# Kernel optimization log

Measured on AMD Instinct MI355X. Metric: run time of the kernel, lower is better.

## Reference

```python
import jax, jax.numpy as jnp
import numpy as np


def setup_inputs() -> dict:
    key = jax.random.key(0)
    ks = jax.random.split(key, 7)
    B, T, H = 4, 4096, 1024
    scale = 1.0 / np.sqrt(H)
    states = jax.random.normal(ks[0], (B, T, H), dtype=jnp.float32)
    Wq = jax.random.normal(ks[1], (H, H), dtype=jnp.float32) * scale
    bq = jax.random.normal(ks[2], (H,), dtype=jnp.float32) * 0.01
    Wk = jax.random.normal(ks[3], (H, H), dtype=jnp.float32) * scale
    bk = jax.random.normal(ks[4], (H,), dtype=jnp.float32) * 0.01
    Wv = jax.random.normal(ks[5], (H, H), dtype=jnp.float32) * scale
    bv = jax.random.normal(ks[6], (H,), dtype=jnp.float32) * 0.01
    return {"states": states, "Wq": Wq, "bq": bq, "Wk": Wk, "bk": bk,
            "Wv": Wv, "bv": bv, "window": 8}


def reference(states, Wq, bq, Wk, bk, Wv, bv, window):
    # states: [B, T, H]; torch Linear: y = x @ W.T + b
    B, T, H = states.shape
    W = window + 1  # context length per query (positions t-window .. t)
    q = states @ Wq.T + bq  # [B,T,H]
    k = states @ Wk.T + bk
    v = states @ Wv.T + bv
    # Windowed gather indices: idx[t, w] = t - window + w
    idx = jnp.arange(T)[:, None] + jnp.arange(-window, 1)[None, :]  # [T,W]
    valid = idx >= 0
    idxc = jnp.clip(idx, 0, T - 1)
    kw = k[:, idxc]  # [B,T,W,H]
    vw = v[:, idxc]  # [B,T,W,H]
    scores = jnp.einsum('bth,btwh->btw', q, kw) / jnp.sqrt(jnp.float32(H))
    scores = jnp.where(valid[None, :, :], scores, -jnp.inf)
    attn = jax.nn.softmax(scores, axis=-1)  # [B,T,W]
    out = jnp.einsum('btw,btwh->bth', attn, vw)
    return out
```

## Files before the change

### kernel.cpp

```cpp
#include <hip/hip_runtime.h>
#include <hip/hip_bf16.h>
#include <stdint.h>
#include <math.h>

typedef __attribute__((ext_vector_type(8))) short short8;
typedef __attribute__((ext_vector_type(4))) float f32x4;

#define H_DIM 1024
#define T_SEQ 4096
#define BM 128
#define BN 128
#define BK 32

static __device__ __forceinline__ float bf2f(unsigned short u) {
  union { unsigned int i; float f; } c;
  c.i = ((unsigned int)u) << 16;
  return c.f;
}

static __device__ __forceinline__ unsigned short f2bf(float f) {
  __hip_bfloat16 h = __float2bfloat16(f);
  unsigned short u;
  __builtin_memcpy(&u, &h, 2);
  return u;
}

static __device__ __forceinline__ void gload16(const void* g, void* l) {
  __builtin_amdgcn_global_load_lds(
      (const __attribute__((address_space(1))) void*)g,
      (__attribute__((address_space(3))) void*)l,
      16, 0, 0);
}

__global__ __launch_bounds__(256) void cvt_kernel(
    const float* __restrict__ in, __hip_bfloat16* __restrict__ out, int n8)
{
  int i = blockIdx.x * blockDim.x + threadIdx.x;
  const int stride = gridDim.x * blockDim.x;
  for (; i < n8; i += stride) {
    const float4* p = (const float4*)in + (size_t)i * 2;
    float4 a = p[0], b = p[1];
    short8 o;
    o[0] = (short)f2bf(a.x); o[1] = (short)f2bf(a.y);
    o[2] = (short)f2bf(a.z); o[3] = (short)f2bf(a.w);
    o[4] = (short)f2bf(b.x); o[5] = (short)f2bf(b.y);
    o[6] = (short)f2bf(b.z); o[7] = (short)f2bf(b.w);
    ((short8*)out)[i] = o;
  }
}

__global__ __launch_bounds__(256) void cvt3_kernel(
    const float* __restrict__ i0, const float* __restrict__ i1,
    const float* __restrict__ i2,
    __hip_bfloat16* __restrict__ o0, __hip_bfloat16* __restrict__ o1,
    __hip_bfloat16* __restrict__ o2, int n8)
{
  const float* in = (blockIdx.y == 0) ? i0 : ((blockIdx.y == 1) ? i1 : i2);
  __hip_bfloat16* out = (blockIdx.y == 0) ? o0 : ((blockIdx.y == 1) ? o1 : o2);
  int i = blockIdx.x * blockDim.x + threadIdx.x;
  const int stride = gridDim.x * blockDim.x;
  for (; i < n8; i += stride) {
    const float4* p = (const float4*)in + (size_t)i * 2;
    float4 a = p[0], b = p[1];
    short8 o;
    o[0] = (short)f2bf(a.x); o[1] = (short)f2bf(a.y);
    o[2] = (short)f2bf(a.z); o[3] = (short)f2bf(a.w);
    o[4] = (short)f2bf(b.x); o[5] = (short)f2bf(b.y);
    o[6] = (short)f2bf(b.z); o[7] = (short)f2bf(b.w);
    ((short8*)out)[i] = o;
  }
}

__global__ __launch_bounds__(256) void qkv_gemm_kernel(
    const __hip_bfloat16* __restrict__ X,
    const __hip_bfloat16* __restrict__ Wq,
    const __hip_bfloat16* __restrict__ Wk,
    const __hip_bfloat16* __restrict__ Wv,
    const float* __restrict__ bq,
    const float* __restrict__ bk,
    const float* __restrict__ bv,
    __hip_bfloat16* __restrict__ Qo,
    __hip_bfloat16* __restrict__ Ko,
    __hip_bfloat16* __restrict__ Vo,
    int M)
{
  __shared__ __hip_bfloat16 sA[BM * BK];
  __shared__ __hip_bfloat16 sB[BN * BK];

  const int m0 = blockIdx.x * BM;
  const int ytile = blockIdx.y;
  const int which = ytile >> 3;
  const int n_local = (ytile & 7) * BN;

  const __hip_bfloat16* Wsel = (which == 0) ? Wq : ((which == 1) ? Wk : Wv);
  const float* Bsel          = (which == 0) ? bq : ((which == 1) ? bk : bv);
  __hip_bfloat16* Osel       = (which == 0) ? Qo : ((which == 1) ? Ko : Vo);

  const int tid  = threadIdx.x;
  const int lane = tid & 63;
  const int wv   = tid >> 6;
  const int wm   = (wv >> 1) * 64;
  const int wn   = (wv & 1) * 64;

  f32x4 acc[4][4];
  #pragma unroll
  for (int i = 0; i < 4; ++i)
    #pragma unroll
    for (int j = 0; j < 4; ++j)
      acc[i][j] = (f32x4){0.f, 0.f, 0.f, 0.f};

  const int ar = wm + (lane & 15);
  const int br = wn + (lane & 15);
  const int kq = lane >> 4;

  const int nkt = H_DIM / BK;

  for (int kt = 0; kt < nkt; ++kt) {
    const int k0 = kt * BK;
    #pragma unroll
    for (int i = 0; i < 2; ++i) {
      int idx = i * 256 + tid;
      int row = idx >> 2;
      int ck  = (idx & 3) * 8;
      gload16(X    + (size_t)(m0 + row)      * H_DIM + k0 + ck, (char*)sA + idx * 16);
      gload16(Wsel + (size_t)(n_local + row) * H_DIM + k0 + ck, (char*)sB + idx * 16);
    }
    __syncthreads();

    const short8* pA = (const short8*)sA;
    const short8* pB = (const short8*)sB;
    short8 afrag[4], bfrag[4];
    #pragma unroll
    for (int mi = 0; mi < 4; ++mi)
      afrag[mi] = pA[(ar + mi * 16) * 4 + kq];
    #pragma unroll
    for (int ni = 0; ni < 4; ++ni)
      bfrag[ni] = pB[(br + ni * 16) * 4 + kq];

    #pragma unroll
    for (int mi = 0; mi < 4; ++mi)
      #pragma unroll
      for (int ni = 0; ni < 4; ++ni)
        acc[mi][ni] = __builtin_amdgcn_mfma_f32_16x16x32_bf16(
            afrag[mi], bfrag[ni], acc[mi][ni], 0, 0, 0);

    __syncthreads();
  }

  #pragma unroll
  for (int ni = 0; ni < 4; ++ni) {
    const int col = n_local + wn + ni * 16 + (lane & 15);
    const float bias = Bsel[col];
    #pragma unroll
    for (int mi = 0; mi < 4; ++mi) {
      const int rowbase = m0 + wm + mi * 16 + (lane >> 4) * 4;
      #pragma unroll
      for (int r = 0; r < 4; ++r) {
        float v = acc[mi][ni][r] + bias;
        Osel[(size_t)(rowbase + r) * H_DIM + col] = __float2bfloat16(v);
      }
    }
  }
}

__global__ __launch_bounds__(256) void local_attn_kernel(
    const __hip_bfloat16* __restrict__ Q,
    const __hip_bfloat16* __restrict__ Km,
    const __hip_bfloat16* __restrict__ V,
    const int* __restrict__ winp,
    float* __restrict__ Out,
    int M)
{
  const int row = (int)((blockIdx.x * blockDim.x + threadIdx.x) >> 6);
  if (row >= M) return;
  const int lane = threadIdx.x & 63;
  const int t = row & (T_SEQ - 1);
  const int Wn = *winp;
  const float scale = 0.03125f;

  const size_t base = (size_t)row * H_DIM + (size_t)lane * 16;

  float q[16];
  {
    const short8* p = (const short8*)(Q + base);
    short8 a = p[0], b = p[1];
    #pragma unroll
    for (int j = 0; j < 8; ++j) {
      q[j]     = bf2f((unsigned short)a[j]);
      q[8 + j] = bf2f((unsigned short)b[j]);
    }
  }

  if (Wn == 8) {
    float sc[9];
    #pragma unroll
    for (int w = 0; w < 9; ++w) {
      const int dt = 8 - w;
      float s = -INFINITY;
      if (t - dt >= 0) {
        const short8* kp = (const short8*)(Km + base - (size_t)dt * H_DIM);
        short8 ka = kp[0], kb = kp[1];
        float d = 0.f;
        #pragma unroll
        for (int j = 0; j < 8; ++j) {
          d += q[j]     * bf2f((unsigned short)ka[j]);
          d += q[8 + j] * bf2f((unsigned short)kb[j]);
        }
        #pragma unroll
        for (int off = 32; off >= 1; off >>= 1) d += __shfl_xor(d, off, 64);
        s = d * scale;
      }
      sc[w] = s;
    }
    float m = sc[0];
    #pragma unroll
    for (int w = 1; w < 9; ++w) m = fmaxf(m, sc[w]);
    float l = 0.f;
    #pragma unroll
    for (int w = 0; w < 9; ++w) { sc[w] = __expf(sc[w] - m); l += sc[w]; }
    const float inv = 1.f / l;

    float o[16];
    #pragma unroll
    for (int j = 0; j < 16; ++j) o[j] = 0.f;
    #pragma unroll
    for (int w = 0; w < 9; ++w) {
      const int dt = 8 - w;
      if (t - dt >= 0) {
        const short8* vp = (const short8*)(V + base - (size_t)dt * H_DIM);
        short8 va = vp[0], vb = vp[1];
        const float aw = sc[w] * inv;
        #pragma unroll
        for (int j = 0; j < 8; ++j) {
          o[j]     += aw * bf2f((unsigned short)va[j]);
          o[8 + j] += aw * bf2f((unsigned short)vb[j]);
        }
      }
    }

    float4* op = (float4*)(Out + base);
    op[0] = (float4){o[0],  o[1],  o[2],  o[3]};
    op[1] = (float4){o[4],  o[5],  o[6],  o[7]};
    op[2] = (float4){o[8],  o[9],  o[10], o[11]};
    op[3] = (float4){o[12], o[13], o[14], o[15]};
  } else {
    float m = -INFINITY, l = 0.f;
    float o[16];
    #pragma unroll
    for (int j = 0; j < 16; ++j) o[j] = 0.f;
    for (int w = 0; w <= Wn; ++w) {
      const int dt = Wn - w;
      if (t - dt < 0) continue;
      const short8* kp = (const short8*)(Km + base - (size_t)dt * H_DIM);
      short8 ka = kp[0], kb = kp[1];
      float d = 0.f;
      #pragma unroll
      for (int j = 0; j < 8; ++j) {
        d += q[j]     * bf2f((unsigned short)ka[j]);
        d += q[8 + j] * bf2f((unsigned short)kb[j]);
      }
      #pragma unroll
      for (int off = 32; off >= 1; off >>= 1) d += __shfl_xor(d, off, 64);
      const float s = d * scale;
      const float mn = fmaxf(m, s);
      const float corr = (m == -INFINITY) ? 0.f : __expf(m - mn);
      const float p = __expf(s - mn);
      l = l * corr + p;
      const short8* vp = (const short8*)(V + base - (size_t)dt * H_DIM);
      short8 va = vp[0], vb = vp[1];
      #pragma unroll
      for (int j = 0; j < 8; ++j) {
        o[j]     = o[j]     * corr + p * bf2f((unsigned short)va[j]);
        o[8 + j] = o[8 + j] * corr + p * bf2f((unsigned short)vb[j]);
      }
      m = mn;
    }
    const float inv = 1.f / l;
    float4* op = (float4*)(Out + base);
    op[0] = (float4){o[0]  * inv, o[1]  * inv, o[2]  * inv, o[3]  * inv};
    op[1] = (float4){o[4]  * inv, o[5]  * inv, o[6]  * inv, o[7]  * inv};
    op[2] = (float4){o[8]  * inv, o[9]  * inv, o[10] * inv, o[11] * inv};
    op[3] = (float4){o[12] * inv, o[13] * inv, o[14] * inv, o[15] * inv};
  }
}

extern "C" void kernel_launch(void* const* d_in, const int* in_sizes, int n_in,
                              void* d_out, int out_size, void* d_ws, size_t ws_size,
                              hipStream_t stream) {
  const float* X  = (const float*)d_in[0];
  const float* Wq = (const float*)d_in[1];
  const float* bq = (const float*)d_in[2];
  const float* Wk = (const float*)d_in[3];
  const float* bk = (const float*)d_in[4];
  const float* Wv = (const float*)d_in[5];
  const float* bv = (const float*)d_in[6];
  const int* winp = (const int*)d_in[7];

  const int M = in_sizes[0] / H_DIM;
  const size_t MH = (size_t)M * H_DIM;
  const size_t HH = (size_t)H_DIM * H_DIM;

  __hip_bfloat16* Xb  = (__hip_bfloat16*)d_ws;
  __hip_bfloat16* Wqb = Xb  + MH;
  __hip_bfloat16* Wkb = Wqb + HH;
  __hip_bfloat16* Wvb = Wkb + HH;
  __hip_bfloat16* Qb  = Wvb + HH;
  __hip_bfloat16* Kb  = Qb  + MH;
  __hip_bfloat16* Vb  = Kb  + MH;
  float* Out = (float*)d_out;

  cvt_kernel<<<2048, 256, 0, stream>>>(X, Xb, (int)(MH / 8));
  cvt3_kernel<<<dim3(512, 3), 256, 0, stream>>>(Wq, Wk, Wv, Wqb, Wkb, Wvb,
                                                (int)(HH / 8));

  dim3 g1(M / BM, 3 * (H_DIM / BN));
  qkv_gemm_kernel<<<g1, 256, 0, stream>>>(Xb, Wqb, Wkb, Wvb, bq, bk, bv,
                                          Qb, Kb, Vb, M);

  const int blocks = M / 4;
  local_attn_kernel<<<blocks, 256, 0, stream>>>(Qb, Kb, Vb, winp, Out, M);
}
```

Baseline: 312.7 us.

## Reuse K/V rows across consecutive queries with a register ring buffer

Each wave now handles a chunk of 16 consecutive query rows and keeps the last 9 K and V rows in a register ring buffer. Each new row's K/V is loaded once instead of being reloaded by up to 9 different waves, which cuts global and L2 traffic for the window gather. In exchange register pressure rises sharply (9x2 short8 for each of K and V), launch_bounds is set to 1 block per SM, and there are 16x fewer waves, so latency hiding and occupancy may suffer.

```diff
diff --git a/kernel.cpp b/kernel.cpp
--- a/kernel.cpp
+++ b/kernel.cpp
@@ -11,6 +11,7 @@
 #define BM 128
 #define BN 128
 #define BK 32
+#define CHUNK 16
 
 static __device__ __forceinline__ float bf2f(unsigned short u) {
   union { unsigned int i; float f; } c;
@@ -163,7 +164,113 @@
   }
 }
 
-__global__ __launch_bounds__(256) void local_attn_kernel(
+static __device__ __forceinline__ float dot16(const float* q,
+                                              const short8& a, const short8& b) {
+  float d = 0.f;
+  #pragma unroll
+  for (int e = 0; e < 8; ++e) d += q[e] * bf2f((unsigned short)a[e]);
+  #pragma unroll
+  for (int e = 0; e < 8; ++e) d += q[8 + e] * bf2f((unsigned short)b[e]);
+  return d;
+}
+
+template<bool EDGE>
+static __device__ __forceinline__ void attn_chunk(
+    const __hip_bfloat16* __restrict__ Q,
+    const __hip_bfloat16* __restrict__ Km,
+    const __hip_bfloat16* __restrict__ V,
+    float* __restrict__ Out,
+    int row0, int lane)
+{
+  const float scale = 0.03125f;
+  const size_t lanoff = (size_t)lane * 16;
+
+  short8 kr[9][2];
+  short8 vr[9][2];
+
+  #pragma unroll
+  for (int j = 0; j < 8; ++j) {
+    if (EDGE) {
+      short8 z = {0, 0, 0, 0, 0, 0, 0, 0};
+      kr[j][0] = z; kr[j][1] = z;
+      vr[j][0] = z; vr[j][1] = z;
+    } else {
+      const size_t rb = (size_t)(row0 - 8 + j) * H_DIM + lanoff;
+      const short8* kp = (const short8*)(Km + rb);
+      kr[j][0] = kp[0]; kr[j][1] = kp[1];
+      const short8* vp = (const short8*)(V + rb);
+      vr[j][0] = vp[0]; vr[j][1] = vp[1];
+    }
+  }
+
+  #pragma unroll
+  for (int i = 0; i < CHUNK; ++i) {
+    const size_t rb = (size_t)(row0 + i) * H_DIM + lanoff;
+
+    {
+      const int snew = (i + 8) % 9;
+      const short8* kp = (const short8*)(Km + rb);
+      kr[snew][0] = kp[0]; kr[snew][1] = kp[1];
+      const short8* vp = (const short8*)(V + rb);
+      vr[snew][0] = vp[0]; vr[snew][1] = vp[1];
+    }
+
+    float q[16];
+    {
+      const short8* p = (const short8*)(Q + rb);
+      short8 a = p[0], b = p[1];
+      #pragma unroll
+      for (int e = 0; e < 8; ++e) {
+        q[e]     = bf2f((unsigned short)a[e]);
+        q[8 + e] = bf2f((unsigned short)b[e]);
+      }
+    }
+
+    float sc[9];
+    #pragma unroll
+    for (int j = 0; j < 9; ++j) {
+      const int s = (i + j) % 9;
+      if (EDGE && (i - 8 + j < 0)) {
+        sc[j] = -INFINITY;
+      } else {
+        float d = dot16(q, kr[s][0], kr[s][1]);
+        #pragma unroll
+        for (int off = 32; off >= 1; off >>= 1) d += __shfl_xor(d, off, 64);
+        sc[j] = d * scale;
+      }
+    }
+
+    float m = sc[0];
+    #pragma unroll
+    for (int j = 1; j < 9; ++j) m = fmaxf(m, sc[j]);
+    float l = 0.f;
+    #pragma unroll
+    for (int j = 0; j < 9; ++j) { sc[j] = __expf(sc[j] - m); l += sc[j]; }
+    const float inv = 1.f / l;
+
+    float o[16];
+    #pragma unroll
+    for (int e = 0; e < 16; ++e) o[e] = 0.f;
+    #pragma unroll
+    for (int j = 0; j < 9; ++j) {
+      const int s = (i + j) % 9;
+      const float aw = sc[j] * inv;
+      #pragma unroll
+      for (int e = 0; e < 8; ++e) {
+        o[e]     += aw * bf2f((unsigned short)vr[s][0][e]);
+        o[8 + e] += aw * bf2f((unsigned short)vr[s][1][e]);
+      }
+    }
+
+    float4* op = (float4*)(Out + rb);
+    op[0] = (float4){o[0],  o[1],  o[2],  o[3]};
+    op[1] = (float4){o[4],  o[5],  o[6],  o[7]};
+    op[2] = (float4){o[8],  o[9],  o[10], o[11]};
+    op[3] = (float4){o[12], o[13], o[14], o[15]};
+  }
+}
+
+__global__ __launch_bounds__(256, 1) void local_attn_ring_kernel(
     const __hip_bfloat16* __restrict__ Q,
     const __hip_bfloat16* __restrict__ Km,
     const __hip_bfloat16* __restrict__ V,
@@ -171,94 +278,47 @@
     float* __restrict__ Out,
     int M)
 {
-  const int row = (int)((blockIdx.x * blockDim.x + threadIdx.x) >> 6);
-  if (row >= M) return;
+  const int wave = (int)((blockIdx.x * blockDim.x + threadIdx.x) >> 6);
   const int lane = threadIdx.x & 63;
-  const int t = row & (T_SEQ - 1);
+  const int row0 = wave * CHUNK;
+  if (row0 >= M) return;
+  const int t0 = row0 & (T_SEQ - 1);
   const int Wn = *winp;
+
+  if (Wn == 8) {
+    if (t0 == 0) attn_chunk<true >(Q, Km, V, Out, row0, lane);
+    else         attn_chunk<false>(Q, Km, V, Out, row0, lane);
+    return;
+  }
+
   const float scale = 0.03125f;
-
-  const size_t base = (size_t)row * H_DIM + (size_t)lane * 16;
-
-  float q[16];
-  {
-    const short8* p = (const short8*)(Q + base);
-    short8 a = p[0], b = p[1];
-    #pragma unroll
-    for (int j = 0; j < 8; ++j) {
-      q[j]     = bf2f((unsigned short)a[j]);
-      q[8 + j] = bf2f((unsigned short)b[j]);
-    }
-  }
-
-  if (Wn == 8) {
-    float sc[9];
-    #pragma unroll
-    for (int w = 0; w < 9; ++w) {
-      const int dt = 8 - w;
-      float s = -INFINITY;
-      if (t - dt >= 0) {
-        const short8* kp = (const short8*)(Km + base - (size_t)dt * H_DIM);
-        short8 ka = kp[0], kb = kp[1];
-        float d = 0.f;
-        #pragma unroll
-        for (int j = 0; j < 8; ++j) {
-          d += q[j]     * bf2f((unsigned short)ka[j]);
-          d += q[8 + j] * bf2f((unsigned short)kb[j]);
-        }
-        #pragma unroll
-        for (int off = 32; off >= 1; off >>= 1) d += __shfl_xor(d, off, 64);
-        s = d * scale;
-      }
-      sc[w] = s;
-    }
-    float m = sc[0];
-    #pragma unroll
-    for (int w = 1; w < 9; ++w) m = fmaxf(m, sc[w]);
-    float l = 0.f;
-    #pragma unroll
-    for (int w = 0; w < 9; ++w) { sc[w] = __expf(sc[w] - m); l += sc[w]; }
-    const float inv = 1.f / l;
-
-    float o[16];
-    #pragma unroll
-    for (int j = 0; j < 16; ++j) o[j] = 0.f;
-    #pragma unroll
-    for (int w = 0; w < 9; ++w) {
-      const int dt = 8 - w;
-      if (t - dt >= 0) {
-        const short8* vp = (const short8*)(V + base - (size_t)dt * H_DIM);
-        short8 va = vp[0], vb = vp[1];
-        const float aw = sc[w] * inv;
-        #pragma unroll
-        for (int j = 0; j < 8; ++j) {
-          o[j]     += aw * bf2f((unsigned short)va[j]);
-          o[8 + j] += aw * bf2f((unsigned short)vb[j]);
-        }
-      }
-    }
-
-    float4* op = (float4*)(Out + base);
-    op[0] = (float4){o[0],  o[1],  o[2],  o[3]};
-    op[1] = (float4){o[4],  o[5],  o[6],  o[7]};
-    op[2] = (float4){o[8],  o[9],  o[10], o[11]};
-    op[3] = (float4){o[12], o[13], o[14], o[15]};
-  } else {
+  for (int i = 0; i < CHUNK; ++i) {
+    const int row = row0 + i;
+    const int t = row & (T_SEQ - 1);
+    const size_t rb = (size_t)row * H_DIM + (size_t)lane * 16;
+
+    float q[16];
+    {
+      const short8* p = (const short8*)(Q + rb);
+      short8 a = p[0], b = p[1];
+      #pragma unroll
+      for (int e = 0; e < 8; ++e) {
+        q[e]     = bf2f((unsigned short)a[e]);
+        q[8 + e] = bf2f((unsigned short)b[e]);
+      }
+    }
+
     float m = -INFINITY, l = 0.f;
     float o[16];
     #pragma unroll
-    for (int j = 0; j < 16; ++j) o[j] = 0.f;
+    for (int e = 0; e < 16; ++e) o[e] = 0.f;
     for (int w = 0; w <= Wn; ++w) {
       const int dt = Wn - w;
       if (t - dt < 0) continue;
-      const short8* kp = (const short8*)(Km + base - (size_t)dt * H_DIM);
-      short8 ka = kp[0], kb = kp[1];
-      float d = 0.f;
-      #pragma unroll
-      for (int j = 0; j < 8; ++j) {
-        d += q[j]     * bf2f((unsigned short)ka[j]);
-        d += q[8 + j] * bf2f((unsigned short)kb[j]);
-      }
+      const size_t kb = rb - (size_t)dt * H_DIM;
+      const short8* kp = (const short8*)(Km + kb);
+      short8 ka = kp[0], kb8 = kp[1];
+      float d = dot16(q, ka, kb8);
       #pragma unroll
       for (int off = 32; off >= 1; off >>= 1) d += __shfl_xor(d, off, 64);
       const float s = d * scale;
@@ -266,17 +326,17 @@
       const float corr = (m == -INFINITY) ? 0.f : __expf(m - mn);
       const float p = __expf(s - mn);
       l = l * corr + p;
-      const short8* vp = (const short8*)(V + base - (size_t)dt * H_DIM);
+      const short8* vp = (const short8*)(V + kb);
       short8 va = vp[0], vb = vp[1];
       #pragma unroll
-      for (int j = 0; j < 8; ++j) {
-        o[j]     = o[j]     * corr + p * bf2f((unsigned short)va[j]);
-        o[8 + j] = o[8 + j] * corr + p * bf2f((unsigned short)vb[j]);
+      for (int e = 0; e < 8; ++e) {
+        o[e]     = o[e]     * corr + p * bf2f((unsigned short)va[e]);
+        o[8 + e] = o[8 + e] * corr + p * bf2f((unsigned short)vb[e]);
       }
       m = mn;
     }
     const float inv = 1.f / l;
-    float4* op = (float4*)(Out + base);
+    float4* op = (float4*)(Out + rb);
     op[0] = (float4){o[0]  * inv, o[1]  * inv, o[2]  * inv, o[3]  * inv};
     op[1] = (float4){o[4]  * inv, o[5]  * inv, o[6]  * inv, o[7]  * inv};
     op[2] = (float4){o[8]  * inv, o[9]  * inv, o[10] * inv, o[11] * inv};
@@ -317,6 +377,7 @@
   qkv_gemm_kernel<<<g1, 256, 0, stream>>>(Xb, Wqb, Wkb, Wvb, bq, bk, bv,
                                           Qb, Kb, Vb, M);
 
-  const int blocks = M / 4;
-  local_attn_kernel<<<blocks, 256, 0, stream>>>(Qb, Kb, Vb, winp, Out, M);
-}
+  const int waves = M / CHUNK;
+  const int blocks = (waves + 3) / 4;
+  local_attn_ring_kernel<<<blocks, 256, 0, stream>>>(Qb, Kb, Vb, winp, Out, M);
+}
```

New measurement: 452.4 us. +44.7%, slower.

## Rewrite QKV GEMM as 256x256 tile, 8-wave, double-buffered pipelined kernel

Applied to the files above, without the earlier changes.

Replaces the 128x128x32 single-buffered QKV GEMM with a 256x256x64 tile kernel using 512 threads, double-buffered swizzled LDS, and interleaved global-to-LDS staging between MFMA phases with setprio. The aim is to hide global load latency, remove LDS bank conflicts, and raise arithmetic intensity per LDS byte. The cost is one block per CU with 128KB of LDS, plus intricate manual vmcnt and barrier choreography that is fragile to get right.

```diff
diff --git a/kernel.cpp b/kernel.cpp
--- a/kernel.cpp
+++ b/kernel.cpp
@@ -8,9 +8,6 @@
 
 #define H_DIM 1024
 #define T_SEQ 4096
-#define BM 128
-#define BN 128
-#define BK 32
 
 static __device__ __forceinline__ float bf2f(unsigned short u) {
   union { unsigned int i; float f; } c;
@@ -31,6 +28,10 @@
       (__attribute__((address_space(3))) void*)l,
       16, 0, 0);
 }
+
+#define FENCE asm volatile("" ::: "memory")
+#define BAR   __builtin_amdgcn_s_barrier()
+#define LGKM0 asm volatile("s_waitcnt lgkmcnt(0)" ::: "memory")
 
 __global__ __launch_bounds__(256) void cvt_kernel(
     const float* __restrict__ in, __hip_bfloat16* __restrict__ out, int n8)
@@ -71,7 +72,34 @@
   }
 }
 
-__global__ __launch_bounds__(256) void qkv_gemm_kernel(
+#define GNT 16
+
+static __device__ __forceinline__ void stage_half(
+    const __hip_bfloat16* __restrict__ G, int grow0, int k0, char* dstHalf,
+    int tid)
+{
+  const int w = tid >> 6, l = tid & 63;
+  #pragma unroll
+  for (int r = 0; r < 2; ++r) {
+    const int D = (r * 8 + w) * 1024 + l * 16;
+    const int L = D ^ (((D >> 7) & 7) << 4);
+    const int row = L >> 7;
+    const int cb  = L & 127;
+    const char* src = (const char*)G + (size_t)(grow0 + row) * (H_DIM * 2)
+                      + k0 * 2 + cb;
+    gload16(src, dstHalf + D);
+  }
+}
+
+static __device__ __forceinline__ short8 lds_frag(const char* half, int row,
+                                                  int ksub, int kq)
+{
+  int a = row * 128 + ksub * 64 + kq * 16;
+  a ^= ((row & 7) << 4);
+  return *(const short8*)(half + a);
+}
+
+__global__ __launch_bounds__(512, 1) void qkv_gemm8_kernel(
     const __hip_bfloat16* __restrict__ X,
     const __hip_bfloat16* __restrict__ Wq,
     const __hip_bfloat16* __restrict__ Wk,
@@ -84,13 +112,12 @@
     __hip_bfloat16* __restrict__ Vo,
     int M)
 {
-  __shared__ __hip_bfloat16 sA[BM * BK];
-  __shared__ __hip_bfloat16 sB[BN * BK];
-
-  const int m0 = blockIdx.x * BM;
+  __shared__ char lds[131072];
+
+  const int m0 = blockIdx.x * 256;
   const int ytile = blockIdx.y;
-  const int which = ytile >> 3;
-  const int n_local = (ytile & 7) * BN;
+  const int which = ytile >> 2;
+  const int nb = (ytile & 3) * 256;
 
   const __hip_bfloat16* Wsel = (which == 0) ? Wq : ((which == 1) ? Wk : Wv);
   const float* Bsel          = (which == 0) ? bq : ((which == 1) ? bk : bv);
@@ -98,62 +125,126 @@
 
   const int tid  = threadIdx.x;
   const int lane = tid & 63;
-  const int wv   = tid >> 6;
-  const int wm   = (wv >> 1) * 64;
-  const int wn   = (wv & 1) * 64;
-
-  f32x4 acc[4][4];
+  const int wid  = tid >> 6;
+  const int wr   = wid >> 2;
+  const int wc   = wid & 3;
+  const int lrow = lane & 15;
+  const int kq   = lane >> 4;
+
+  #define AHALF(b, h) (lds + (b) * 65536 + (h) * 16384)
+  #define BHALF(b, h) (lds + (b) * 65536 + 32768 + (h) * 16384)
+
+  f32x4 acc[8][4];
   #pragma unroll
-  for (int i = 0; i < 4; ++i)
+  for (int i = 0; i < 8; ++i)
     #pragma unroll
     for (int j = 0; j < 4; ++j)
       acc[i][j] = (f32x4){0.f, 0.f, 0.f, 0.f};
 
-  const int ar = wm + (lane & 15);
-  const int br = wn + (lane & 15);
-  const int kq = lane >> 4;
-
-  const int nkt = H_DIM / BK;
-
-  for (int kt = 0; kt < nkt; ++kt) {
-    const int k0 = kt * BK;
-    #pragma unroll
-    for (int i = 0; i < 2; ++i) {
-      int idx = i * 256 + tid;
-      int row = idx >> 2;
-      int ck  = (idx & 3) * 8;
-      gload16(X    + (size_t)(m0 + row)      * H_DIM + k0 + ck, (char*)sA + idx * 16);
-      gload16(Wsel + (size_t)(n_local + row) * H_DIM + k0 + ck, (char*)sB + idx * 16);
-    }
-    __syncthreads();
-
-    const short8* pA = (const short8*)sA;
-    const short8* pB = (const short8*)sB;
-    short8 afrag[4], bfrag[4];
-    #pragma unroll
-    for (int mi = 0; mi < 4; ++mi)
-      afrag[mi] = pA[(ar + mi * 16) * 4 + kq];
-    #pragma unroll
-    for (int ni = 0; ni < 4; ++ni)
-      bfrag[ni] = pB[(br + ni * 16) * 4 + kq];
-
-    #pragma unroll
-    for (int mi = 0; mi < 4; ++mi)
-      #pragma unroll
-      for (int ni = 0; ni < 4; ++ni)
-        acc[mi][ni] = __builtin_amdgcn_mfma_f32_16x16x32_bf16(
-            afrag[mi], bfrag[ni], acc[mi][ni], 0, 0, 0);
-
-    __syncthreads();
+  stage_half(Wsel, nb +   0, 0,  BHALF(0, 0), tid);
+  stage_half(Wsel, nb + 128, 0,  BHALF(0, 1), tid);
+  stage_half(X,    m0 +   0, 0,  AHALF(0, 0), tid);
+  stage_half(X,    m0 + 128, 0,  AHALF(0, 1), tid);
+  stage_half(Wsel, nb +   0, 64, BHALF(1, 0), tid);
+  stage_half(Wsel, nb + 128, 64, BHALF(1, 1), tid);
+  asm volatile("s_waitcnt vmcnt(4)" ::: "memory");
+  BAR;
+
+  short8 aF[4][2];
+  short8 bF[4][2];
+
+  for (int t = 0; t < GNT; ++t) {
+    const int cur = t & 1, nxt = cur ^ 1;
+    const char* myA = AHALF(cur, wr);
+    const char* myB = BHALF(cur, wc >> 1);
+    const int rB0 = (wc & 1) * 64;
+
+    #pragma unroll
+    for (int mi = 0; mi < 4; ++mi)
+      #pragma unroll
+      for (int ks = 0; ks < 2; ++ks)
+        aF[mi][ks] = lds_frag(myA, mi * 16 + lrow, ks, kq);
+    #pragma unroll
+    for (int ni = 0; ni < 2; ++ni)
+      #pragma unroll
+      for (int ks = 0; ks < 2; ++ks)
+        bF[ni][ks] = lds_frag(myB, rB0 + ni * 16 + lrow, ks, kq);
+    if (t + 1 < GNT) stage_half(X, m0 + 0, (t + 1) * 64, AHALF(nxt, 0), tid);
+    FENCE; BAR; LGKM0; __builtin_amdgcn_sched_barrier(0);
+    __builtin_amdgcn_s_setprio(1);
+    #pragma unroll
+    for (int mi = 0; mi < 4; ++mi)
+      #pragma unroll
+      for (int ni = 0; ni < 2; ++ni)
+        #pragma unroll
+        for (int ks = 0; ks < 2; ++ks)
+          acc[mi][ni] = __builtin_amdgcn_mfma_f32_16x16x32_bf16(
+              aF[mi][ks], bF[ni][ks], acc[mi][ni], 0, 0, 0);
+    __builtin_amdgcn_s_setprio(0);
+    FENCE; BAR;
+
+    #pragma unroll
+    for (int ni = 2; ni < 4; ++ni)
+      #pragma unroll
+      for (int ks = 0; ks < 2; ++ks)
+        bF[ni][ks] = lds_frag(myB, rB0 + ni * 16 + lrow, ks, kq);
+    if (t + 1 < GNT) stage_half(X, m0 + 128, (t + 1) * 64, AHALF(nxt, 1), tid);
+    FENCE; BAR; LGKM0; __builtin_amdgcn_sched_barrier(0);
+    __builtin_amdgcn_s_setprio(1);
+    #pragma unroll
+    for (int mi = 0; mi < 4; ++mi)
+      #pragma unroll
+      for (int ni = 2; ni < 4; ++ni)
+        #pragma unroll
+        for (int ks = 0; ks < 2; ++ks)
+          acc[mi][ni] = __builtin_amdgcn_mfma_f32_16x16x32_bf16(
+              aF[mi][ks], bF[ni][ks], acc[mi][ni], 0, 0, 0);
+    __builtin_amdgcn_s_setprio(0);
+    FENCE; BAR;
+
+    #pragma unroll
+    for (int mi = 0; mi < 4; ++mi)
+      #pragma unroll
+      for (int ks = 0; ks < 2; ++ks)
+        aF[mi][ks] = lds_frag(myA, (mi + 4) * 16 + lrow, ks, kq);
+    if (t + 2 < GNT) stage_half(Wsel, nb + 0, (t + 2) * 64, BHALF(cur, 0), tid);
+    FENCE; BAR; LGKM0; __builtin_amdgcn_sched_barrier(0);
+    __builtin_amdgcn_s_setprio(1);
+    #pragma unroll
+    for (int mi = 0; mi < 4; ++mi)
+      #pragma unroll
+      for (int ni = 0; ni < 2; ++ni)
+        #pragma unroll
+        for (int ks = 0; ks < 2; ++ks)
+          acc[mi + 4][ni] = __builtin_amdgcn_mfma_f32_16x16x32_bf16(
+              aF[mi][ks], bF[ni][ks], acc[mi + 4][ni], 0, 0, 0);
+    __builtin_amdgcn_s_setprio(0);
+    FENCE; BAR;
+
+    if (t + 2 < GNT) stage_half(Wsel, nb + 128, (t + 2) * 64, BHALF(cur, 1), tid);
+    FENCE;
+    __builtin_amdgcn_s_setprio(1);
+    #pragma unroll
+    for (int mi = 0; mi < 4; ++mi)
+      #pragma unroll
+      for (int ni = 2; ni < 4; ++ni)
+        #pragma unroll
+        for (int ks = 0; ks < 2; ++ks)
+          acc[mi + 4][ni] = __builtin_amdgcn_mfma_f32_16x16x32_bf16(
+              aF[mi][ks], bF[ni][ks], acc[mi + 4][ni], 0, 0, 0);
+    __builtin_amdgcn_s_setprio(0);
+    if (t + 2 < GNT) { asm volatile("s_waitcnt vmcnt(4)" ::: "memory"); }
+    else             { asm volatile("s_waitcnt vmcnt(0)" ::: "memory"); }
+    FENCE; BAR;
   }
 
   #pragma unroll
   for (int ni = 0; ni < 4; ++ni) {
-    const int col = n_local + wn + ni * 16 + (lane & 15);
+    const int col = nb + wc * 64 + ni * 16 + lrow;
     const float bias = Bsel[col];
     #pragma unroll
-    for (int mi = 0; mi < 4; ++mi) {
-      const int rowbase = m0 + wm + mi * 16 + (lane >> 4) * 4;
+    for (int mi = 0; mi < 8; ++mi) {
+      const int rowbase = m0 + wr * 128 + mi * 16 + kq * 4;
       #pragma unroll
       for (int r = 0; r < 4; ++r) {
         float v = acc[mi][ni][r] + bias;
@@ -161,6 +252,8 @@
       }
     }
   }
+  #undef AHALF
+  #undef BHALF
 }
 
 __global__ __launch_bounds__(256) void local_attn_kernel(
@@ -313,9 +406,9 @@
   cvt3_kernel<<<dim3(512, 3), 256, 0, stream>>>(Wq, Wk, Wv, Wqb, Wkb, Wvb,
                                                 (int)(HH / 8));
 
-  dim3 g1(M / BM, 3 * (H_DIM / BN));
-  qkv_gemm_kernel<<<g1, 256, 0, stream>>>(Xb, Wqb, Wkb, Wvb, bq, bk, bv,
-                                          Qb, Kb, Vb, M);
+  dim3 g1(M / 256, 12);
+  qkv_gemm8_kernel<<<g1, 512, 0, stream>>>(Xb, Wqb, Wkb, Wvb, bq, bk, bv,
+                                           Qb, Kb, Vb, M);
 
   const int blocks = M / 4;
   local_attn_kernel<<<blocks, 256, 0, stream>>>(Qb, Kb, Vb, winp, Out, M);
```

New measurement: 292.2 us. 1.07x faster.
